# Performance work log

Measured on AMD Instinct MI355X. Metric: run time of the kernel, lower is better.

## Reference

```python
import jax, jax.numpy as jnp
import numpy as np

D_MODEL = 256
NUM_HEADS = 8
WINDOW = 7
B, H, W = 2, 56, 56


def setup_inputs() -> dict:
    key = jax.random.key(0)
    ks = jax.random.split(key, 9)
    s = D_MODEL ** -0.5
    return {
        "x": jax.random.normal(ks[0], (B, D_MODEL, H, W), jnp.float32),
        "wq": jax.random.normal(ks[1], (D_MODEL, D_MODEL), jnp.float32) * s,
        "bq": jnp.zeros((D_MODEL,), jnp.float32),
        "wk": jax.random.normal(ks[2], (D_MODEL, D_MODEL), jnp.float32) * s,
        "bk": jnp.zeros((D_MODEL,), jnp.float32),
        "wv": jax.random.normal(ks[3], (D_MODEL, D_MODEL), jnp.float32) * s,
        "bv": jnp.zeros((D_MODEL,), jnp.float32),
        "wo": jax.random.normal(ks[4], (D_MODEL, D_MODEL), jnp.float32) * s,
        "bo": jnp.zeros((D_MODEL,), jnp.float32),
    }


def _proj(x, w, b):
    # 1x1 conv == channel matmul. x: [B,C,H,W], w: [Cout,Cin], b: [Cout]
    return jnp.einsum('oc,bchw->bohw', w, x) + b[None, :, None, None]


def _windows(t, ws):
    # t: [B,h,d,H,W] -> [B,h,d,H,W,ws*ws], zero-padded sliding windows.
    # Row-major (i*ws + j) flattening matches torch unfold(3).unfold(4).view(...,-1).
    pad = ws // 2
    Hh, Ww = t.shape[-2], t.shape[-1]
    tp = jnp.pad(t, ((0, 0), (0, 0), (0, 0), (pad, pad), (pad, pad)))
    return jnp.stack([tp[..., i:i + Hh, j:j + Ww]
                      for i in range(ws) for j in range(ws)], axis=-1)


def reference(x, wq, bq, wk, bk, wv, bv, wo, bo):
    Bt, C, Hh, Ww = x.shape
    hd = C // NUM_HEADS
    scale = hd ** -0.5
    q = _proj(x, wq, bq).reshape(Bt, NUM_HEADS, hd, Hh, Ww)
    k = _proj(x, wk, bk).reshape(Bt, NUM_HEADS, hd, Hh, Ww)
    v = _proj(x, wv, bv).reshape(Bt, NUM_HEADS, hd, Hh, Ww)
    kw = _windows(k, WINDOW)  # [B,h,d,H,W,ws^2]
    vw = _windows(v, WINDOW)
    attn = jnp.einsum('bhdxy,bhdxyw->bhxyw', q, kw) * scale
    attn = jax.nn.softmax(attn, axis=-1)
    out = jnp.einsum('bhxyw,bhdxyw->bhdxy', attn, vw).reshape(Bt, C, Hh, Ww)
    return _proj(out, wo, bo)
```

## Files before the change

kernel.cpp:

```cpp
#include <hip/hip_runtime.h>
#include <hip/hip_bf16.h>
#include <cstdint>

#define NHEAD 8
#define HD 32
#define DM 256
#define HH 56
#define WWID 56
#define HW 3136
#define NB 2
#define SCALE 0.17677669529663687f

typedef _Float16 f16;
typedef __attribute__((ext_vector_type(2))) _Float16 f16x2;
typedef __attribute__((ext_vector_type(8))) _Float16 f16x8;
typedef __attribute__((ext_vector_type(4))) float floatx4;

union U16 { uint4 u; f16x2 h2[4]; f16 h[8]; };

__global__ __launch_bounds__(256) void prep(
    const float* __restrict__ x,
    const float* __restrict__ wq, const float* __restrict__ wk,
    const float* __restrict__ wv, const float* __restrict__ wo,
    f16* __restrict__ xT, f16* __restrict__ wcat, f16* __restrict__ wob)
{
    const int bid = blockIdx.x;
    const int t = threadIdx.x;
    if (bid < 1568) {
        __shared__ float tile[32][33];
        const int b = bid / 784, r = bid - 784 * b;
        const int ct = r / 98;
        const int p0 = (r - ct * 98) * 32, c0 = ct * 32;
        const int tx = t & 31, ty = t >> 5;
        const float* xb = x + (size_t)b * DM * HW;
        #pragma unroll
        for (int i = 0; i < 4; ++i)
            tile[ty + i * 8][tx] = xb[(size_t)(c0 + ty + i * 8) * HW + p0 + tx];
        __syncthreads();
        f16* xo = xT + (size_t)b * HW * DM;
        #pragma unroll
        for (int i = 0; i < 4; ++i)
            xo[(size_t)(p0 + ty + i * 8) * DM + c0 + tx] =
                (f16)tile[tx][ty + i * 8];
    } else {
        const int gid = (bid - 1568) * 256 + t;
        const int idx4 = gid << 2;
        const int sel = idx4 >> 16;
        const int off = idx4 & 65535;
        const float* src = sel == 0 ? wq : (sel == 1 ? wk : (sel == 2 ? wv : wo));
        f16* dst = sel < 3 ? (wcat + (sel << 16) + off) : (wob + off);
        float4 f = *(const float4*)&src[off];
        union { ushort4 u; f16 h[4]; } pk;
        pk.h[0] = (f16)f.x; pk.h[1] = (f16)f.y;
        pk.h[2] = (f16)f.z; pk.h[3] = (f16)f.w;
        *(ushort4*)dst = pk.u;
    }
}

template<int MODE>
__global__ __launch_bounds__(256) void gemm_mfma(
    const f16* __restrict__ A,
    const f16* __restrict__ Bm,
    const float* __restrict__ b0, const float* __restrict__ b1,
    const float* __restrict__ b2,
    void* __restrict__ o0, void* __restrict__ o1, void* __restrict__ o2)
{
    const int bb = blockIdx.z;
    const int n0 = blockIdx.x * 64;
    const int m0 = blockIdx.y * 128;
    const f16* Bb = Bm + (size_t)bb * HW * DM + (size_t)n0 * DM;

    __shared__ __align__(16) f16 As[128][40];
    __shared__ __align__(16) f16 Bs[64][40];

    const int t = threadIdx.x;
    const int wave = t >> 6, lane = t & 63;
    const int quad = lane >> 4, l16 = lane & 15;
    const int mw = (wave & 1) * 64, nw = (wave >> 1) * 32;

    floatx4 acc[4][2] = {};

    const int am = t >> 2, ak = (t & 3) << 3;
    const int bn = t >> 2, bk = (t & 3) << 3;

    for (int k0g = 0; k0g < DM; k0g += 32) {
        *(uint4*)&As[am][ak]      = *(const uint4*)&A[(size_t)(m0 + am) * DM + k0g + ak];
        *(uint4*)&As[am + 64][ak] = *(const uint4*)&A[(size_t)(m0 + am + 64) * DM + k0g + ak];
        *(uint4*)&Bs[bn][bk]      = *(const uint4*)&Bb[(size_t)bn * DM + k0g + bk];
        __syncthreads();
        f16x8 af[4], bf[2];
        #pragma unroll
        for (int mt = 0; mt < 4; ++mt)
            af[mt] = *(const f16x8*)&As[mw + mt * 16 + l16][quad * 8];
        #pragma unroll
        for (int nt = 0; nt < 2; ++nt)
            bf[nt] = *(const f16x8*)&Bs[nw + nt * 16 + l16][quad * 8];
        #pragma unroll
        for (int mt = 0; mt < 4; ++mt)
            #pragma unroll
            for (int nt = 0; nt < 2; ++nt)
                acc[mt][nt] = __builtin_amdgcn_mfma_f32_16x16x32_f16(
                    af[mt], bf[nt], acc[mt][nt], 0, 0, 0);
        __syncthreads();
    }

    if (MODE == 0) {
        #pragma unroll
        for (int mt = 0; mt < 4; ++mt) {
            const int gm = m0 + mw + mt * 16 + quad * 4;
            const int proj = gm >> 8;
            const int c = gm & 255;
            const int h = c >> 5, d0 = c & 31;
            const float* bptr = proj == 0 ? b0 : (proj == 1 ? b1 : b2);
            f16* op = (f16*)(proj == 0 ? o0 : (proj == 1 ? o1 : o2));
            const float sc = proj == 0 ? SCALE : 1.0f;
            const size_t base = ((size_t)(bb * NHEAD + h) * HW) * HD + d0;
            float bias[4] = {bptr[c], bptr[c + 1], bptr[c + 2], bptr[c + 3]};
            #pragma unroll
            for (int nt = 0; nt < 2; ++nt) {
                const int p = n0 + nw + nt * 16 + l16;
                union { ushort4 u; f16 h[4]; } pk;
                #pragma unroll
                for (int r = 0; r < 4; ++r)
                    pk.h[r] = (f16)((acc[mt][nt][r] + bias[r]) * sc);
                *(ushort4*)&op[base + (size_t)p * HD] = pk.u;
            }
        }
    } else {
        float* yo = (float*)o0;
        #pragma unroll
        for (int mt = 0; mt < 4; ++mt) {
            const int gc = m0 + mw + mt * 16 + quad * 4;
            #pragma unroll
            for (int r = 0; r < 4; ++r) {
                const float bias = b0[gc + r];
                #pragma unroll
                for (int nt = 0; nt < 2; ++nt) {
                    const int p = n0 + nw + nt * 16 + l16;
                    yo[(size_t)(bb * DM + gc + r) * HW + p] = acc[mt][nt][r] + bias;
                }
            }
        }
    }
}

#define HROWS 8
#define HPOS  (HROWS * WWID)
#define HPP   (HPOS + 6)

__global__ __launch_bounds__(448) void attn_win(
    const f16* __restrict__ q,
    const f16* __restrict__ k,
    const f16* __restrict__ v,
    f16* __restrict__ out)
{
    __shared__ uint4 kh[HPP * 4];
    __shared__ uint4 vh[HPP * 4];

    const int t = threadIdx.x;
    const int tile = blockIdx.x;
    const int h = blockIdx.y, b = blockIdx.z;
    const int y0 = tile * 2;
    const size_t base = (size_t)(b * NHEAD + h) * HW * HD;
    const f16* kp = k + base;
    const f16* vp = v + base;

    #pragma unroll
    for (int it = 0; it < 4; ++it) {
        const int u = t + it * 448;
        const int pos = u >> 2, ch = u & 3;
        const int hr = pos / WWID;
        const int gx = pos - hr * WWID;
        const int gy = y0 - 3 + hr;
        uint4 kv = make_uint4(0, 0, 0, 0), vv = make_uint4(0, 0, 0, 0);
        if ((unsigned)gy < HH) {
            const size_t g = (size_t)(gy * WWID + gx) * HD + (ch << 3);
            kv = *(const uint4*)&kp[g];
            vv = *(const uint4*)&vp[g];
        }
        kh[u + 12] = kv;
        vh[u + 12] = vv;
    }
    if (t < 48) {
        const int ps = t % 6;
        const int fi = (ps < 3 ? ps * 4 : (HPOS + ps) * 4) + ((t / 6) & 3);
        const uint4 z = make_uint4(0, 0, 0, 0);
        if (t < 24) kh[fi] = z; else vh[fi] = z;
    }
    __syncthreads();

    const int pl = t >> 2;
    const int ch = t & 3;
    const int lx = pl >= WWID ? pl - WWID : pl;
    const int p = y0 * WWID + pl;

    U16 qu;
    qu.u = *(const uint4*)(q + base + (size_t)p * HD + (ch << 3));

    const uint4* kb4 = kh + t;
    const uint4* vb4 = vh + t;

    float of[8] = {};
    float sum = 0.f;
    for (int i = 0; i < 7; ++i) {
        #pragma unroll
        for (int j = 0; j < 7; ++j) {
            const int off4 = (i * WWID + j) << 2;
            U16 ku; ku.u = kb4[off4];
            float s;
            s = __builtin_amdgcn_fdot2(ku.h2[0], qu.h2[0], 0.0f, false);
            s = __builtin_amdgcn_fdot2(ku.h2[1], qu.h2[1], s, false);
            s = __builtin_amdgcn_fdot2(ku.h2[2], qu.h2[2], s, false);
            s = __builtin_amdgcn_fdot2(ku.h2[3], qu.h2[3], s, false);
            s += __shfl_xor(s, 1);
            s += __shfl_xor(s, 2);
            const bool xv = (unsigned)(lx + j - 3) < WWID;
            const float e = __expf(s);
            sum += xv ? e : 1.0f;
            const float wt = xv ? e : 0.0f;
            U16 vu; vu.u = vb4[off4];
            of[0] = fmaf((float)vu.h[0], wt, of[0]);
            of[1] = fmaf((float)vu.h[1], wt, of[1]);
            of[2] = fmaf((float)vu.h[2], wt, of[2]);
            of[3] = fmaf((float)vu.h[3], wt, of[3]);
            of[4] = fmaf((float)vu.h[4], wt, of[4]);
            of[5] = fmaf((float)vu.h[5], wt, of[5]);
            of[6] = fmaf((float)vu.h[6], wt, of[6]);
            of[7] = fmaf((float)vu.h[7], wt, of[7]);
        }
    }

    const float inv = 1.0f / sum;
    f16* op = out + ((size_t)b * HW + p) * DM + h * HD + (ch << 3);
    U16 ou;
    #pragma unroll
    for (int j = 0; j < 8; ++j)
        ou.h[j] = (f16)(of[j] * inv);
    *(uint4*)op = ou.u;
}

extern "C" void kernel_launch(void* const* d_in, const int* in_sizes, int n_in,
                              void* d_out, int out_size, void* d_ws, size_t ws_size,
                              hipStream_t stream) {
    const float* x  = (const float*)d_in[0];
    const float* wq = (const float*)d_in[1];
    const float* bq = (const float*)d_in[2];
    const float* wk = (const float*)d_in[3];
    const float* bk = (const float*)d_in[4];
    const float* wv = (const float*)d_in[5];
    const float* bv = (const float*)d_in[6];
    const float* wo = (const float*)d_in[7];
    const float* bo = (const float*)d_in[8];
    float* out = (float*)d_out;

    const size_t NPC = (size_t)NB * HW * DM;
    f16* xT    = (f16*)d_ws;
    f16* wcat  = xT + NPC;
    f16* wob   = wcat + 768 * 256;
    f16* qb    = wob + 256 * 256;
    f16* kb    = qb + NPC;
    f16* vb    = kb + NPC;
    f16* attnT = vb + NPC;

    prep<<<1824, 256, 0, stream>>>(x, wq, wk, wv, wo, xT, wcat, wob);
    gemm_mfma<0><<<dim3(HW / 64, 6, NB), 256, 0, stream>>>(
        wcat, xT, bq, bk, bv, qb, kb, vb);
    attn_win<<<dim3(28, NHEAD, NB), 448, 0, stream>>>(qb, kb, vb, attnT);
    gemm_mfma<1><<<dim3(HW / 64, 2, NB), 256, 0, stream>>>(
        wob, attnT, bo, bo, bo, out, out, out);
}
```

Measured before the change: 110.3 us.

## Use async global-to-LDS GEMM loads, DPP quad reductions, and exp2-based softmax

The GEMM tile staging now goes through global_load_lds, which copies straight from global memory into LDS. This drops the register round trip and the LDS padding. In the attention loop, the shuffle-based quad sum becomes DPP moves. The exponent moves to exp2 with log2e folded into the Q scale, padded-column weights use precomputed masks with a constant sum offset, and the final division becomes a hardware reciprocal. Removing the LDS padding may add bank conflicts on the fragment reads, and the reciprocal trades a little precision for speed.

Result: faster. 106.6 us (-3.3%).

```diff
diff --git a/kernel.cpp b/kernel.cpp
--- a/kernel.cpp
+++ b/kernel.cpp
@@ -1,5 +1,4 @@
 #include <hip/hip_runtime.h>
-#include <hip/hip_bf16.h>
 #include <cstdint>
 
 #define NHEAD 8
@@ -11,12 +10,41 @@
 #define NB 2
 #define SCALE 0.17677669529663687f
 
+#if __has_builtin(__builtin_amdgcn_exp2f)
+#define QSCALE 0.25503488f
+#define EXPW(x) __builtin_amdgcn_exp2f(x)
+#else
+#define QSCALE SCALE
+#define EXPW(x) __expf(x)
+#endif
+
 typedef _Float16 f16;
 typedef __attribute__((ext_vector_type(2))) _Float16 f16x2;
 typedef __attribute__((ext_vector_type(8))) _Float16 f16x8;
 typedef __attribute__((ext_vector_type(4))) float floatx4;
 
 union U16 { uint4 u; f16x2 h2[4]; f16 h[8]; };
+
+#define GLD16(g, l) __builtin_amdgcn_global_load_lds( \
+    (__attribute__((address_space(1))) void*)(g),     \
+    (__attribute__((address_space(3))) void*)(l), 16, 0, 0)
+
+#if __has_builtin(__builtin_amdgcn_update_dpp)
+__device__ __forceinline__ float quad_sum(float s) {
+    float t1 = __int_as_float(__builtin_amdgcn_update_dpp(
+        0, __float_as_int(s), 0xB1, 0xF, 0xF, true));
+    s += t1;
+    float t2 = __int_as_float(__builtin_amdgcn_update_dpp(
+        0, __float_as_int(s), 0x4E, 0xF, 0xF, true));
+    return s + t2;
+}
+#else
+__device__ __forceinline__ float quad_sum(float s) {
+    s += __shfl_xor(s, 1);
+    s += __shfl_xor(s, 2);
+    return s;
+}
+#endif
 
 __global__ __launch_bounds__(256) void prep(
     const float* __restrict__ x,
@@ -70,8 +98,8 @@
     const int m0 = blockIdx.y * 128;
     const f16* Bb = Bm + (size_t)bb * HW * DM + (size_t)n0 * DM;
 
-    __shared__ __align__(16) f16 As[128][40];
-    __shared__ __align__(16) f16 Bs[64][40];
+    __shared__ __align__(16) f16 As[128][32];
+    __shared__ __align__(16) f16 Bs[64][32];
 
     const int t = threadIdx.x;
     const int wave = t >> 6, lane = t & 63;
@@ -80,13 +108,18 @@
 
     floatx4 acc[4][2] = {};
 
-    const int am = t >> 2, ak = (t & 3) << 3;
-    const int bn = t >> 2, bk = (t & 3) << 3;
-
-    for (int k0g = 0; k0g < DM; k0g += 32) {
-        *(uint4*)&As[am][ak]      = *(const uint4*)&A[(size_t)(m0 + am) * DM + k0g + ak];
-        *(uint4*)&As[am + 64][ak] = *(const uint4*)&A[(size_t)(m0 + am + 64) * DM + k0g + ak];
-        *(uint4*)&Bs[bn][bk]      = *(const uint4*)&Bb[(size_t)bn * DM + k0g + bk];
+    const int sr = t >> 2;
+    const int sq = (t & 3) << 3;
+    const f16* gA = A + (size_t)(m0 + sr) * DM + sq;
+    const f16* gB = Bb + (size_t)sr * DM + sq;
+    f16* lA  = &As[sr][sq];
+    f16* lA2 = &As[sr + 64][sq];
+    f16* lB  = &Bs[sr][sq];
+
+    for (int k0 = 0; k0 < DM; k0 += 32) {
+        GLD16(gA + k0, lA);
+        GLD16(gA + 64 * DM + k0, lA2);
+        GLD16(gB + k0, lB);
         __syncthreads();
         f16x8 af[4], bf[2];
         #pragma unroll
@@ -113,7 +146,7 @@
             const int h = c >> 5, d0 = c & 31;
             const float* bptr = proj == 0 ? b0 : (proj == 1 ? b1 : b2);
             f16* op = (f16*)(proj == 0 ? o0 : (proj == 1 ? o1 : o2));
-            const float sc = proj == 0 ? SCALE : 1.0f;
+            const float sc = proj == 0 ? QSCALE : 1.0f;
             const size_t base = ((size_t)(bb * NHEAD + h) * HW) * HD + d0;
             float bias[4] = {bptr[c], bptr[c + 1], bptr[c + 2], bptr[c + 3]};
             #pragma unroll
@@ -200,8 +233,14 @@
     const uint4* kb4 = kh + t;
     const uint4* vb4 = vh + t;
 
+    float wm[7];
+    #pragma unroll
+    for (int j = 0; j < 7; ++j)
+        wm[j] = ((unsigned)(lx + j - 3) < WWID) ? 1.0f : 0.0f;
+    const int nin = (lx < 3 ? 3 - lx : 0) + (lx > 52 ? lx - 52 : 0);
+
     float of[8] = {};
-    float sum = 0.f;
+    float sum = (float)(7 * nin);
     for (int i = 0; i < 7; ++i) {
         #pragma unroll
         for (int j = 0; j < 7; ++j) {
@@ -212,12 +251,10 @@
             s = __builtin_amdgcn_fdot2(ku.h2[1], qu.h2[1], s, false);
             s = __builtin_amdgcn_fdot2(ku.h2[2], qu.h2[2], s, false);
             s = __builtin_amdgcn_fdot2(ku.h2[3], qu.h2[3], s, false);
-            s += __shfl_xor(s, 1);
-            s += __shfl_xor(s, 2);
-            const bool xv = (unsigned)(lx + j - 3) < WWID;
-            const float e = __expf(s);
-            sum += xv ? e : 1.0f;
-            const float wt = xv ? e : 0.0f;
+            s = quad_sum(s);
+            const float e = EXPW(s);
+            const float wt = e * wm[j];
+            sum += wt;
             U16 vu; vu.u = vb4[off4];
             of[0] = fmaf((float)vu.h[0], wt, of[0]);
             of[1] = fmaf((float)vu.h[1], wt, of[1]);
@@ -230,7 +267,11 @@
         }
     }
 
+#if __has_builtin(__builtin_amdgcn_rcpf)
+    const float inv = __builtin_amdgcn_rcpf(sum);
+#else
     const float inv = 1.0f / sum;
+#endif
     f16* op = out + ((size_t)b * HW + p) * DM + h * HD + (ch << 3);
     U16 ou;
     #pragma unroll
```
